# Performance work log

Hardware: AMD Instinct MI355X
Metric: run time of the kernel (lower is better)

The kernel has to match this reference:

```python
import jax, jax.numpy as jnp
import numpy as np

SIGMA = 1.0


def setup_inputs() -> dict:
    key = jax.random.key(0)
    k1, k2 = jax.random.split(key)
    B, N = 32, 1024
    logits = jax.random.normal(k1, (B, N, 1), dtype=jnp.float32)
    labels = jax.random.randint(k2, (B, N, 1), 0, 5).astype(jnp.float32)
    item_mask = jnp.ones((B, N), dtype=bool)
    return {"logits": logits, "labels": labels, "item_mask": item_mask}


def _ndcg_weights(y, sorted_indices):
    # y: (B, N) relevance labels; sorted_indices: (B, N) argsort of scores desc
    b, n = y.shape
    gains = 2.0 ** y - 1.0                                   # (B, N)
    ideal_sorted = -jnp.sort(-gains, axis=-1)                # descending sort
    positions = jnp.arange(1, n + 1, dtype=y.dtype)          # (N,)
    discounts = 1.0 / jnp.log2(positions + 1.0)              # (N,)  (k=None)
    idcg = jnp.clip((ideal_sorted * discounts).sum(-1, keepdims=True), 1e-8)
    # scatter: ranks[b, sorted_indices[b, j]] = j + 1
    ranks = jnp.zeros_like(y).at[jnp.arange(b)[:, None], sorted_indices].set(
        jnp.broadcast_to(positions, (b, n)))
    disc_i = 1.0 / jnp.log2(ranks + 1.0)                     # (B, N)
    gain_diff = jnp.abs(gains[:, :, None] - gains[:, None, :])   # (B, N, N)
    disc_diff = jnp.abs(disc_i[:, :, None] - disc_i[:, None, :]) # (B, N, N)
    return gain_diff * disc_diff / idcg[..., None]


def reference(logits, labels, item_mask):
    scores = logits[..., 0]                                  # (B, N)
    y = labels[..., 0].astype(jnp.float32)                   # (B, N)
    n = scores.shape[1]
    sorted_indices = jnp.argsort(-jax.lax.stop_gradient(scores), axis=-1)
    s_ij = SIGMA * (scores[:, :, None] - scores[:, None, :])     # (B, N, N)
    y_ij = jnp.sign(y[:, :, None] - y[:, None, :])               # (B, N, N)
    weights = _ndcg_weights(y, sorted_indices)                   # (B, N, N)
    pair_loss = jax.nn.softplus(-y_ij * s_ij) * weights          # log1p(exp(.))
    triu = jnp.triu(jnp.ones((n, n), dtype=bool), k=1)
    valid = item_mask[:, :, None] & item_mask[:, None, :]
    pair_loss = pair_loss * triu[None] * valid
    loss = pair_loss.sum(axis=(1, 2))                            # (B,)
    return loss.mean()                                           # reduction='mean'
```

## Files before the change

kernel.cpp:

```cpp
#include <hip/hip_runtime.h>
#include <math.h>


#define N 1024
#define PC 8
#define IC 32
#define ROWS_PB 32
#define JPT 4

__global__ __launch_bounds__(256) void lrank_prep(const float* __restrict__ logits,
                                                  const float* __restrict__ labels,
                                                  float* __restrict__ disc,
                                                  float* __restrict__ idcg,
                                                  float* __restrict__ out)
{
    __shared__ float sh_s[N];
    __shared__ int   cntb[256];
    __shared__ float redp[256];
    __shared__ int   hist[5];

    const int b = blockIdx.y;
    const int c = blockIdx.x;
    const int t = threadIdx.x;
    const float* sb = logits + b * N;

    ((float4*)sh_s)[t] = ((const float4*)sb)[t];
    if (t < 5) hist[t] = 0;
    __syncthreads();

    const int r  = c * 128 + (t & 127);
    const int h  = t >> 7;
    const int j0 = h * 512;
    const float si = sh_s[r];
    int cnt = 0;
    for (int jj = 0; jj < 512; jj += 4) {
        const float4 sv = ((float4*)sh_s)[(j0 + jj) >> 2];
        const int j = j0 + jj;
        cnt += (sv.x > si) || (sv.x == si && (j + 0) < r);
        cnt += (sv.y > si) || (sv.y == si && (j + 1) < r);
        cnt += (sv.z > si) || (sv.z == si && (j + 2) < r);
        cnt += (sv.w > si) || (sv.w == si && (j + 3) < r);
    }
    cntb[t] = cnt;
    __syncthreads();
    if (t < 128) {
        const int total = cntb[t] + cntb[t + 128];
        disc[b * N + r] = 1.0f / __log2f((float)(total + 2));
    }

    if (c == 0) {
        const float* yb = labels + b * N;
        const float4 yv = ((const float4*)yb)[t];
        atomicAdd(&hist[(int)yv.x], 1);
        atomicAdd(&hist[(int)yv.y], 1);
        atomicAdd(&hist[(int)yv.z], 1);
        atomicAdd(&hist[(int)yv.w], 1);
        __syncthreads();
        const int c4 = hist[4];
        const int c3 = c4 + hist[3];
        const int c2 = c3 + hist[2];
        const int c1 = c2 + hist[1];
        float ip = 0.0f;
        #pragma unroll
        for (int k = 0; k < 4; ++k) {
            const int p = 4 * t + k;
            const float gain = (p < c4) ? 15.0f : (p < c3) ? 7.0f
                             : (p < c2) ? 3.0f  : (p < c1) ? 1.0f : 0.0f;
            ip += gain / __log2f((float)(p + 2));
        }
        redp[t] = ip;
        __syncthreads();
        for (int off = 128; off; off >>= 1) {
            if (t < off) redp[t] += redp[t + off];
            __syncthreads();
        }
        if (t == 0) {
            idcg[b] = fmaxf(redp[0], 1e-8f);
            if (b == 0) out[0] = 0.0f;
        }
    }
}

__global__ __launch_bounds__(256) void lrank_pairs(const float* __restrict__ logits,
                                                   const float* __restrict__ labels,
                                                   const float* __restrict__ disc,
                                                   const float* __restrict__ idcg,
                                                   float* __restrict__ out,
                                                   float inv_B)
{
    __shared__ float4 sh_i[ROWS_PB];
    __shared__ float  red[256];

    const int b = blockIdx.y;
    const int c = blockIdx.x;
    const int t = threadIdx.x;
    const float* sb = logits + b * N;
    const float* yb = labels + b * N;
    const float* db = disc   + b * N;

    float sj[JPT], gj[JPT], dj[JPT];
    #pragma unroll
    for (int k = 0; k < JPT; ++k) {
        const int j = t + 256 * k;
        sj[k] = sb[j];
        gj[k] = exp2f(yb[j]) - 1.0f;
        dj[k] = db[j];
    }
    if (t < ROWS_PB) {
        const int i = c * ROWS_PB + t;
        sh_i[t] = make_float4(sb[i], exp2f(yb[i]) - 1.0f, db[i], 0.0f);
    }
    __syncthreads();

    float acc = 0.0f;
    #pragma unroll 4
    for (int ii = 0; ii < ROWS_PB; ++ii) {
        const float4 f = sh_i[ii];
        #pragma unroll
        for (int k = 0; k < JPT; ++k) {
            const float ds  = f.x - sj[k];
            const float dg  = f.y - gj[k];
            const float arg = (dg > 0.0f) ? -ds : ds;
            const float sp  = __logf(1.0f + __expf(arg));
            acc += sp * fabsf(dg) * fabsf(f.z - dj[k]);
        }
    }

    red[t] = acc;
    __syncthreads();
    for (int off = 128; off; off >>= 1) {
        if (t < off) red[t] += red[t + off];
        __syncthreads();
    }
    if (t == 0) atomicAdd(out, red[0] * 0.5f * inv_B / idcg[b]);
}

extern "C" void kernel_launch(void* const* d_in, const int* in_sizes, int n_in,
                              void* d_out, int out_size, void* d_ws, size_t ws_size,
                              hipStream_t stream) {
    const float* logits = (const float*)d_in[0];
    const float* labels = (const float*)d_in[1];
    const int B = in_sizes[0] / N;

    float* disc = (float*)d_ws;
    float* idcg = disc + B * N;
    float* out  = (float*)d_out;

    lrank_prep <<<dim3(PC, B), dim3(256), 0, stream>>>(logits, labels, disc, idcg, out);
    lrank_pairs<<<dim3(IC, B), dim3(256), 0, stream>>>(logits, labels, disc, idcg, out,
                                                       1.0f / (float)B);
}
```

Measured before the change: 95.29 us.

## Compute only upper-triangle pairs with balanced row pairing; widen prep grid

The pair kernel now evaluates only j>i pairs instead of the full symmetric N×N matrix and halving, which cuts the transcendental work roughly in half. Rows are paired (r, N-1-r) so each block gets a balanced share of triangle work. Each block stages the full per-item (score, gain, disc) table in shared memory as float4, so j-operands come from LDS rather than registers. The prep kernel is split across twice as many blocks with a 4-way partial count to raise parallelism. Costs are more LDS reads per pair and loop-bound divergence inside each row.

```diff
diff --git a/kernel.cpp b/kernel.cpp
--- a/kernel.cpp
+++ b/kernel.cpp
@@ -3,10 +3,9 @@
 
 
 #define N 1024
-#define PC 8
+#define PC 16
 #define IC 32
-#define ROWS_PB 32
-#define JPT 4
+#define RPPB (512 / IC)
 
 __global__ __launch_bounds__(256) void lrank_prep(const float* __restrict__ logits,
                                                   const float* __restrict__ labels,
@@ -28,12 +27,11 @@
     if (t < 5) hist[t] = 0;
     __syncthreads();
 
-    const int r  = c * 128 + (t & 127);
-    const int h  = t >> 7;
-    const int j0 = h * 512;
+    const int r  = c * 64 + (t & 63);
+    const int j0 = (t >> 6) * 256;
     const float si = sh_s[r];
     int cnt = 0;
-    for (int jj = 0; jj < 512; jj += 4) {
+    for (int jj = 0; jj < 256; jj += 4) {
         const float4 sv = ((float4*)sh_s)[(j0 + jj) >> 2];
         const int j = j0 + jj;
         cnt += (sv.x > si) || (sv.x == si && (j + 0) < r);
@@ -43,9 +41,9 @@
     }
     cntb[t] = cnt;
     __syncthreads();
-    if (t < 128) {
-        const int total = cntb[t] + cntb[t + 128];
-        disc[b * N + r] = 1.0f / __log2f((float)(total + 2));
+    if (t < 64) {
+        const int total = cntb[t] + cntb[t + 64] + cntb[t + 128] + cntb[t + 192];
+        disc[b * N + c * 64 + t] = 1.0f / __log2f((float)(total + 2));
     }
 
     if (c == 0) {
@@ -81,6 +79,15 @@
     }
 }
 
+__device__ __forceinline__ float pair_term(const float4 fi, const float4 fj)
+{
+    const float ds  = fi.x - fj.x;
+    const float dg  = fi.y - fj.y;
+    const float arg = (dg > 0.0f) ? -ds : ds;
+    const float sp  = __logf(1.0f + __expf(arg));
+    return sp * fabsf(dg) * fabsf(fi.z - fj.z);
+}
+
 __global__ __launch_bounds__(256) void lrank_pairs(const float* __restrict__ logits,
                                                    const float* __restrict__ labels,
                                                    const float* __restrict__ disc,
@@ -88,42 +95,31 @@
                                                    float* __restrict__ out,
                                                    float inv_B)
 {
-    __shared__ float4 sh_i[ROWS_PB];
+    __shared__ float4 it[N];
     __shared__ float  red[256];
 
     const int b = blockIdx.y;
     const int c = blockIdx.x;
     const int t = threadIdx.x;
-    const float* sb = logits + b * N;
-    const float* yb = labels + b * N;
-    const float* db = disc   + b * N;
 
-    float sj[JPT], gj[JPT], dj[JPT];
-    #pragma unroll
-    for (int k = 0; k < JPT; ++k) {
-        const int j = t + 256 * k;
-        sj[k] = sb[j];
-        gj[k] = exp2f(yb[j]) - 1.0f;
-        dj[k] = db[j];
-    }
-    if (t < ROWS_PB) {
-        const int i = c * ROWS_PB + t;
-        sh_i[t] = make_float4(sb[i], exp2f(yb[i]) - 1.0f, db[i], 0.0f);
-    }
+    const float4 sv = ((const float4*)(logits + b * N))[t];
+    const float4 yv = ((const float4*)(labels + b * N))[t];
+    const float4 dv = ((const float4*)(disc   + b * N))[t];
+    it[4 * t + 0] = make_float4(sv.x, exp2f(yv.x) - 1.0f, dv.x, 0.0f);
+    it[4 * t + 1] = make_float4(sv.y, exp2f(yv.y) - 1.0f, dv.y, 0.0f);
+    it[4 * t + 2] = make_float4(sv.z, exp2f(yv.z) - 1.0f, dv.z, 0.0f);
+    it[4 * t + 3] = make_float4(sv.w, exp2f(yv.w) - 1.0f, dv.w, 0.0f);
     __syncthreads();
 
     float acc = 0.0f;
-    #pragma unroll 4
-    for (int ii = 0; ii < ROWS_PB; ++ii) {
-        const float4 f = sh_i[ii];
-        #pragma unroll
-        for (int k = 0; k < JPT; ++k) {
-            const float ds  = f.x - sj[k];
-            const float dg  = f.y - gj[k];
-            const float arg = (dg > 0.0f) ? -ds : ds;
-            const float sp  = __logf(1.0f + __expf(arg));
-            acc += sp * fabsf(dg) * fabsf(f.z - dj[k]);
-        }
+    #pragma unroll
+    for (int rp = 0; rp < RPPB; ++rp) {
+        const int r1 = c * RPPB + rp;
+        const int r2 = N - 1 - r1;
+        const float4 f1 = it[r1];
+        const float4 f2 = it[r2];
+        for (int j = r1 + 1 + t; j < N; j += 256) acc += pair_term(f1, it[j]);
+        for (int j = r2 + 1 + t; j < N; j += 256) acc += pair_term(f2, it[j]);
     }
 
     red[t] = acc;
@@ -132,7 +128,7 @@
         if (t < off) red[t] += red[t + off];
         __syncthreads();
     }
-    if (t == 0) atomicAdd(out, red[0] * 0.5f * inv_B / idcg[b]);
+    if (t == 0) atomicAdd(out, red[0] * inv_B / idcg[b]);
 }
 
 extern "C" void kernel_launch(void* const* d_in, const int* in_sizes, int n_in,
```

Measured after the change: 90.33 us. 5.2% less time.
